# Kernel optimization log

Measured on AMD Instinct MI355X. Metric: run time of the kernel, lower is better.

## Reference

```python
import jax, jax.numpy as jnp
import numpy as np

B, N, WIDTH, HEADS = 4, 2048, 1024, 16
HEAD_DIM = WIDTH // HEADS  # 64


def setup_inputs() -> dict:
    key = jax.random.key(0)
    k1, k2, k3 = jax.random.split(key, 3)
    x = jax.random.normal(k1, (B, N, WIDTH), dtype=jnp.float32)
    # Linear weights stored as [in, out] (torch stores [out, in]; math y = x @ W_in_out + b)
    w_qkv = jax.random.normal(k2, (WIDTH, 3 * WIDTH), dtype=jnp.float32) * (1.0 / np.sqrt(WIDTH))
    b_qkv = jnp.zeros((3 * WIDTH,), dtype=jnp.float32)
    w_proj = jax.random.normal(k3, (WIDTH, WIDTH), dtype=jnp.float32) * (1.0 / np.sqrt(WIDTH))
    b_proj = jnp.zeros((WIDTH,), dtype=jnp.float32)
    return {"x": x, "w_qkv": w_qkv, "b_qkv": b_qkv, "w_proj": w_proj, "b_proj": b_proj}


def reference(x, w_qkv, b_qkv, w_proj, b_proj):
    bs, n_ctx, width = x.shape
    qkv = x @ w_qkv + b_qkv                      # [b, n, 3*width]
    attn_ch = HEAD_DIM                            # width // heads
    scale = 1.0 / np.sqrt(np.sqrt(attn_ch))       # 1/sqrt(sqrt(d)) applied to q and k
    qkv = qkv.reshape(bs, n_ctx, HEADS, 3 * attn_ch)
    q, k, v = jnp.split(qkv, 3, axis=-1)          # each [b, n, h, d]
    weight = jnp.einsum('bthc,bshc->bhts', q * scale, k * scale)
    weight = jax.nn.softmax(weight, axis=-1)
    out = jnp.einsum('bhts,bshc->bthc', weight, v).reshape(bs, n_ctx, -1)
    return out @ w_proj + b_proj
```

## Files before the change

kernel.cpp:

```cpp
#include <hip/hip_runtime.h>

typedef __attribute__((ext_vector_type(8))) short bf16x8;
typedef __attribute__((ext_vector_type(4))) float f32x4;
typedef __attribute__((ext_vector_type(8))) unsigned short u16x8;
typedef __attribute__((ext_vector_type(4))) unsigned short u16x4;
typedef __attribute__((ext_vector_type(2))) unsigned u32x2;

__device__ __forceinline__ unsigned short f2bf(float f) {
  unsigned u = __builtin_bit_cast(unsigned, f);
  return (unsigned short)((u + 0x7fffu + ((u >> 16) & 1u)) >> 16);
}

__device__ __forceinline__ unsigned cvt_pk_bf16(float lo, float hi) {
  unsigned r;
  asm("v_cvt_pk_bf16_f32 %0, %1, %2" : "=v"(r) : "v"(lo), "v"(hi));
  return r;
}

__device__ __forceinline__ void gl_lds16(const void* g, void* l) {
  __builtin_amdgcn_global_load_lds((const __attribute__((address_space(1))) unsigned*)g,
                                   (__attribute__((address_space(3))) unsigned*)l, 16, 0, 0);
}

__global__ __launch_bounds__(256) void k_cvt(const float* __restrict__ x,
                                             unsigned short* __restrict__ xb) {
  int i = blockIdx.x * 256 + threadIdx.x;
  const float4* s = (const float4*)x;
  float4 a = s[2 * i], b = s[2 * i + 1];
  u16x8 o;
  o[0] = f2bf(a.x); o[1] = f2bf(a.y); o[2] = f2bf(a.z); o[3] = f2bf(a.w);
  o[4] = f2bf(b.x); o[5] = f2bf(b.y); o[6] = f2bf(b.z); o[7] = f2bf(b.w);
  *(u16x8*)(xb + 8 * (size_t)i) = o;
}

__global__ __launch_bounds__(256) void k_wT(const float* __restrict__ w,
                                            unsigned short* __restrict__ wT,
                                            int Nn, int Kk) {
  __shared__ float tile[32][33];
  const int k0 = blockIdx.x * 32, n0 = blockIdx.y * 32;
  const int t = threadIdx.x;
  const int i = t >> 3, j = (t & 7) * 4;
  float4 v = *(const float4*)(w + (size_t)(k0 + i) * Nn + n0 + j);
  tile[i][j] = v.x; tile[i][j + 1] = v.y; tile[i][j + 2] = v.z; tile[i][j + 3] = v.w;
  __syncthreads();
  const int n = i, k4 = j;
  u16x4 o;
  o[0] = f2bf(tile[k4 + 0][n]); o[1] = f2bf(tile[k4 + 1][n]);
  o[2] = f2bf(tile[k4 + 2][n]); o[3] = f2bf(tile[k4 + 3][n]);
  *(u16x4*)(wT + (size_t)(n0 + n) * Kk + k0 + k4) = o;
}

template <int EPI>
__global__ __launch_bounds__(256) void k_gemm(const unsigned short* __restrict__ A,
                                              const unsigned short* __restrict__ Bt,
                                              const float* __restrict__ bias, int Nx,
                                              int MT,
                                              float* __restrict__ outF,
                                              unsigned short* __restrict__ Qb,
                                              unsigned short* __restrict__ Kb,
                                              unsigned short* __restrict__ Vb) {
  __shared__ unsigned short As[128 * 32];
  __shared__ unsigned short Bs[128 * 32];
  const int t = threadIdx.x;
  const int nwg = gridDim.x;
  const int wg = (blockIdx.x & 7) * (nwg >> 3) + (blockIdx.x >> 3);
  const int brow = (wg % MT) * 128, bcol = (wg / MT) * 128;
  const int lane = t & 63, wid = t >> 6;
  const int wr = (wid >> 1) * 64, wc = (wid & 1) * 64;
  const int g = lane >> 4, qr = lane & 15;
  const f32x4 fzero = {0.f, 0.f, 0.f, 0.f};
  f32x4 acc[4][4];
#pragma unroll
  for (int i = 0; i < 4; ++i)
#pragma unroll
    for (int n = 0; n < 4; ++n) acc[i][n] = fzero;
  const unsigned short* Ag = A + (size_t)(brow + (t >> 2)) * 1024 + (t & 3) * 8;
  const unsigned short* Bg = Bt + (size_t)(bcol + (t >> 2)) * 1024 + (t & 3) * 8;
  unsigned short* Asl = As + t * 8;
  unsigned short* Bsl = Bs + t * 8;
  for (int kt = 0; kt < 32; ++kt) {
    const int k0 = kt * 32;
    gl_lds16(Ag + k0, Asl);
    gl_lds16(Ag + 64 * 1024 + k0, Asl + 2048);
    gl_lds16(Bg + k0, Bsl);
    gl_lds16(Bg + 64 * 1024 + k0, Bsl + 2048);
    __syncthreads();
    bf16x8 a[4], b[4];
#pragma unroll
    for (int i = 0; i < 4; ++i) a[i] = *(const bf16x8*)&As[(wr + i * 16 + qr) * 32 + g * 8];
#pragma unroll
    for (int n = 0; n < 4; ++n) b[n] = *(const bf16x8*)&Bs[(wc + n * 16 + qr) * 32 + g * 8];
#pragma unroll
    for (int i = 0; i < 4; ++i)
#pragma unroll
      for (int n = 0; n < 4; ++n)
        acc[i][n] = __builtin_amdgcn_mfma_f32_16x16x32_bf16(a[i], b[n], acc[i][n], 0, 0, 0);
    __syncthreads();
  }
#pragma unroll
  for (int i = 0; i < 4; ++i) {
#pragma unroll
    for (int n = 0; n < 4; ++n) {
      const int col = bcol + wc + n * 16 + qr;
      const float bv = bias[col];
      float v4[4];
#pragma unroll
      for (int r = 0; r < 4; ++r) v4[r] = acc[i][n][r] + bv;
      const int row0 = brow + wr + i * 16 + g * 4;
      if constexpr (EPI == 0) {
#pragma unroll
        for (int r = 0; r < 4; ++r) outF[(size_t)(row0 + r) * Nx + col] = v4[r];
      } else {
        const int bb = row0 >> 11, tkn0 = row0 & 2047;
        const unsigned c = (unsigned)col;
        const unsigned h = c / 192u;
        const unsigned rem = c - h * 192u;
        const unsigned which = rem >> 6, d = rem & 63u;
        if (which == 2u) {
          u16x4 pk;
#pragma unroll
          for (int r = 0; r < 4; ++r) pk[r] = f2bf(v4[r]);
          *(u16x4*)&Vb[(size_t)(((unsigned)bb * 16u + h) * 64u + d) * 2048u + (unsigned)tkn0] = pk;
        } else {
          const float sc = (which == 0u) ? (0.35355339059327373f * 1.4426950408889634f)
                                         : 0.35355339059327373f;
          unsigned short* dst = (which == 0u) ? Qb : Kb;
#pragma unroll
          for (int r = 0; r < 4; ++r)
            dst[(size_t)(((unsigned)bb * 16u + h) * 2048u + (unsigned)(tkn0 + r)) * 64u + d] =
                f2bf(v4[r] * sc);
        }
      }
    }
  }
}

__global__ __launch_bounds__(512, 4) void k_attn(const unsigned short* __restrict__ Qb,
                                                 const unsigned short* __restrict__ Kb,
                                                 const unsigned short* __restrict__ Vt,
                                                 unsigned short* __restrict__ Ao) {
  __shared__ unsigned short Kl[2][64][64];
  __shared__ unsigned short Vl[2][64][64];
  __shared__ unsigned short Pl[8][2][16][72];
  const int bid = blockIdx.x;
  const int bh = (bid & 7) * 8 + ((bid >> 3) & 7);
  const int qt = bid >> 6;
  const int t = threadIdx.x, lane = t & 63, w = t >> 6;
  const int g = lane >> 4, q = lane & 15;
  const int q0 = qt * 256 + w * 32;
  const unsigned short* Qbase = Qb + ((size_t)bh * 2048 + q0) * 64;
  const char* Kg = (const char*)(Kb + (size_t)bh * 2048 * 64);
  const char* Vg = (const char*)(Vt + (size_t)bh * 64 * 2048);
  const int lr = lane >> 3, lc = lane & 7;
  const int swz = (lc ^ lr) << 4;
  const char* Ksrc = Kg + (size_t)(8 * w + lr) * 128 + swz;
  const char* Vsrc = Vg + (size_t)(8 * w + lr) * 4096 + swz;
  unsigned short* Kd[2], *Vd[2];
  Kd[0] = &Kl[0][8 * w][0] + lane * 8;
  Kd[1] = &Kl[1][8 * w][0] + lane * 8;
  Vd[0] = &Vl[0][8 * w][0] + lane * 8;
  Vd[1] = &Vl[1][8 * w][0] + lane * 8;

#define STAGE(buf, it_)                              \
  do {                                               \
    gl_lds16(Ksrc + (size_t)(it_) * 8192, Kd[buf]);  \
    gl_lds16(Vsrc + (size_t)(it_) * 128, Vd[buf]);   \
  } while (0)

  bf16x8 qf[2][2];
#pragma unroll
  for (int G = 0; G < 2; ++G)
#pragma unroll
    for (int h = 0; h < 2; ++h)
      qf[G][h] = *(const bf16x8*)(Qbase + (size_t)(G * 16 + q) * 64 + h * 32 + g * 8);
  const f32x4 fzero = {0.f, 0.f, 0.f, 0.f};
  f32x4 o0[4], o1[4];
#pragma unroll
  for (int i = 0; i < 4; ++i) { o0[i] = fzero; o1[i] = fzero; }
  float l0 = 0.f, l1 = 0.f;

  STAGE(0, 0);
  __syncthreads();

  for (int it = 0; it < 32; ++it) {
    const int cur = it & 1;
    if (it < 31) STAGE(cur ^ 1, it + 1);
    f32x4 s0[4], s1[4];
    __builtin_amdgcn_s_setprio(1);
#pragma unroll
    for (int kf = 0; kf < 4; ++kf) {
      const int row = kf * 16 + q;
      const char* kp = (const char*)&Kl[cur][row][0];
      const int sw = (row & 7) << 4;
      bf16x8 kaL = *(const bf16x8*)(kp + ((g * 16) ^ sw));
      bf16x8 kaH = *(const bf16x8*)(kp + ((64 + g * 16) ^ sw));
      s0[kf] = __builtin_amdgcn_mfma_f32_16x16x32_bf16(kaL, qf[0][0], fzero, 0, 0, 0);
      s0[kf] = __builtin_amdgcn_mfma_f32_16x16x32_bf16(kaH, qf[0][1], s0[kf], 0, 0, 0);
      s1[kf] = __builtin_amdgcn_mfma_f32_16x16x32_bf16(kaL, qf[1][0], fzero, 0, 0, 0);
      s1[kf] = __builtin_amdgcn_mfma_f32_16x16x32_bf16(kaH, qf[1][1], s1[kf], 0, 0, 0);
    }
    __builtin_amdgcn_s_setprio(0);
    {
      unsigned short* Pw = &Pl[w][0][q][0];
#pragma unroll
      for (int kf = 0; kf < 4; ++kf) {
        const float e0 = __builtin_amdgcn_exp2f(s0[kf][0]);
        const float e1 = __builtin_amdgcn_exp2f(s0[kf][1]);
        const float e2 = __builtin_amdgcn_exp2f(s0[kf][2]);
        const float e3 = __builtin_amdgcn_exp2f(s0[kf][3]);
        l0 += (e0 + e1) + (e2 + e3);
        u32x2 pk;
        pk[0] = cvt_pk_bf16(e0, e1);
        pk[1] = cvt_pk_bf16(e2, e3);
        *(u32x2*)(Pw + (8 * kf + 2 * g) * 2) = pk;
      }
    }
    {
      unsigned short* Pw = &Pl[w][1][q][0];
#pragma unroll
      for (int kf = 0; kf < 4; ++kf) {
        const float e0 = __builtin_amdgcn_exp2f(s1[kf][0]);
        const float e1 = __builtin_amdgcn_exp2f(s1[kf][1]);
        const float e2 = __builtin_amdgcn_exp2f(s1[kf][2]);
        const float e3 = __builtin_amdgcn_exp2f(s1[kf][3]);
        l1 += (e0 + e1) + (e2 + e3);
        u32x2 pk;
        pk[0] = cvt_pk_bf16(e0, e1);
        pk[1] = cvt_pk_bf16(e2, e3);
        *(u32x2*)(Pw + (8 * kf + 2 * g) * 2) = pk;
      }
    }
    asm volatile("" ::: "memory");
    const bf16x8 pa00 = *(const bf16x8*)&Pl[w][0][q][g * 8];
    const bf16x8 pa01 = *(const bf16x8*)&Pl[w][0][q][32 + g * 8];
    const bf16x8 pa10 = *(const bf16x8*)&Pl[w][1][q][g * 8];
    const bf16x8 pa11 = *(const bf16x8*)&Pl[w][1][q][32 + g * 8];
    __builtin_amdgcn_s_setprio(1);
#pragma unroll
    for (int dblk = 0; dblk < 4; ++dblk) {
      const int row = dblk * 16 + q;
      const char* vp = (const char*)&Vl[cur][row][0];
      const int sw = (row & 7) << 4;
      bf16x8 vL = *(const bf16x8*)(vp + ((g * 16) ^ sw));
      bf16x8 vH = *(const bf16x8*)(vp + ((64 + g * 16) ^ sw));
      o0[dblk] = __builtin_amdgcn_mfma_f32_16x16x32_bf16(vL, pa00, o0[dblk], 0, 0, 0);
      o0[dblk] = __builtin_amdgcn_mfma_f32_16x16x32_bf16(vH, pa01, o0[dblk], 0, 0, 0);
      o1[dblk] = __builtin_amdgcn_mfma_f32_16x16x32_bf16(vL, pa10, o1[dblk], 0, 0, 0);
      o1[dblk] = __builtin_amdgcn_mfma_f32_16x16x32_bf16(vH, pa11, o1[dblk], 0, 0, 0);
    }
    __builtin_amdgcn_s_setprio(0);
    __syncthreads();
  }
#undef STAGE
  l0 += __shfl_xor(l0, 16); l0 += __shfl_xor(l0, 32);
  l1 += __shfl_xor(l1, 16); l1 += __shfl_xor(l1, 32);
  const float li0 = 1.0f / l0, li1 = 1.0f / l1;
  const int bb = bh >> 4, hh = bh & 15;
  {
    unsigned short* ob = Ao + ((size_t)bb * 2048 + q0 + q) * 1024 + hh * 64 + 4 * g;
#pragma unroll
    for (int dblk = 0; dblk < 4; ++dblk) {
      u16x4 pk;
#pragma unroll
      for (int r = 0; r < 4; ++r) pk[r] = f2bf(o0[dblk][r] * li0);
      *(u16x4*)(ob + dblk * 16) = pk;
    }
  }
  {
    unsigned short* ob = Ao + ((size_t)bb * 2048 + q0 + 16 + q) * 1024 + hh * 64 + 4 * g;
#pragma unroll
    for (int dblk = 0; dblk < 4; ++dblk) {
      u16x4 pk;
#pragma unroll
      for (int r = 0; r < 4; ++r) pk[r] = f2bf(o1[dblk][r] * li1);
      *(u16x4*)(ob + dblk * 16) = pk;
    }
  }
}

extern "C" void kernel_launch(void* const* d_in, const int* in_sizes, int n_in,
                              void* d_out, int out_size, void* d_ws, size_t ws_size,
                              hipStream_t stream) {
  const float* x = (const float*)d_in[0];
  const float* w_qkv = (const float*)d_in[1];
  const float* b_qkv = (const float*)d_in[2];
  const float* w_proj = (const float*)d_in[3];
  const float* b_proj = (const float*)d_in[4];
  float* out = (float*)d_out;
  char* ws = (char*)d_ws;
  unsigned short* xb = (unsigned short*)(ws);
  unsigned short* wqkvT = (unsigned short*)(ws + 16777216);
  unsigned short* wprojT = (unsigned short*)(ws + 23068672);
  unsigned short* Qb = (unsigned short*)(ws + 25165824);
  unsigned short* Kb = (unsigned short*)(ws + 41943040);
  unsigned short* Vt = (unsigned short*)(ws + 58720256);
  unsigned short* Ao = xb;

  hipLaunchKernelGGL(k_cvt, dim3(4096), dim3(256), 0, stream, x, xb);
  hipLaunchKernelGGL(k_wT, dim3(32, 96), dim3(256), 0, stream, w_qkv, wqkvT, 3072, 1024);
  hipLaunchKernelGGL(k_wT, dim3(32, 32), dim3(256), 0, stream, w_proj, wprojT, 1024, 1024);
  hipLaunchKernelGGL((k_gemm<1>), dim3(1536), dim3(256), 0, stream,
                     xb, wqkvT, b_qkv, 3072, 64, (float*)nullptr, Qb, Kb, Vt);
  hipLaunchKernelGGL(k_attn, dim3(512), dim3(512), 0, stream, Qb, Kb, Vt, Ao);
  hipLaunchKernelGGL((k_gemm<0>), dim3(512), dim3(256), 0, stream,
                     Ao, wprojT, b_proj, 1024, 64, out,
                     (unsigned short*)nullptr, (unsigned short*)nullptr, (unsigned short*)nullptr);
}
```

Measured before the change: 193.0 us.

## Feed softmax probabilities to PV MFMA from registers via 16x16x16 instructions

Removes the per-wave LDS round trip for the probability matrix P. The QK^T accumulator layout is reused directly as the B operand of 16x16x16 bf16 MFMAs, and V is read as 4-element slices matching that layout. This saves LDS writes and reads plus the LDS footprint for P, but doubles the number of PV MFMA issues, which use the older half-K instruction, and drops the priority hints around them.

```diff
diff --git a/kernel.cpp b/kernel.cpp
--- a/kernel.cpp
+++ b/kernel.cpp
@@ -1,6 +1,7 @@
 #include <hip/hip_runtime.h>
 
 typedef __attribute__((ext_vector_type(8))) short bf16x8;
+typedef __attribute__((ext_vector_type(4))) short bf16x4;
 typedef __attribute__((ext_vector_type(4))) float f32x4;
 typedef __attribute__((ext_vector_type(8))) unsigned short u16x8;
 typedef __attribute__((ext_vector_type(4))) unsigned short u16x4;
@@ -15,6 +16,18 @@
   unsigned r;
   asm("v_cvt_pk_bf16_f32 %0, %1, %2" : "=v"(r) : "v"(lo), "v"(hi));
   return r;
+}
+
+__device__ __forceinline__ f32x4 mfma16(bf16x4 a, bf16x4 b, f32x4 c) {
+#if __has_builtin(__builtin_amdgcn_mfma_f32_16x16x16bf16_1k)
+  return __builtin_amdgcn_mfma_f32_16x16x16bf16_1k(a, b, c, 0, 0, 0);
+#elif __has_builtin(__builtin_amdgcn_mfma_f32_16x16x16_bf16)
+  return __builtin_amdgcn_mfma_f32_16x16x16_bf16(a, b, c, 0, 0, 0);
+#else
+  f32x4 d;
+  asm("v_mfma_f32_16x16x16_bf16 %0, %1, %2, %3" : "=v"(d) : "v"(a), "v"(b), "v"(c));
+  return d;
+#endif
 }
 
 __device__ __forceinline__ void gl_lds16(const void* g, void* l) {
@@ -141,7 +154,6 @@
                                                  unsigned short* __restrict__ Ao) {
   __shared__ unsigned short Kl[2][64][64];
   __shared__ unsigned short Vl[2][64][64];
-  __shared__ unsigned short Pl[8][2][16][72];
   const int bid = blockIdx.x;
   const int bh = (bid & 7) * 8 + ((bid >> 3) & 7);
   const int qt = bid >> 6;
@@ -200,55 +212,37 @@
       s1[kf] = __builtin_amdgcn_mfma_f32_16x16x32_bf16(kaH, qf[1][1], s1[kf], 0, 0, 0);
     }
     __builtin_amdgcn_s_setprio(0);
-    {
-      unsigned short* Pw = &Pl[w][0][q][0];
-#pragma unroll
-      for (int kf = 0; kf < 4; ++kf) {
-        const float e0 = __builtin_amdgcn_exp2f(s0[kf][0]);
-        const float e1 = __builtin_amdgcn_exp2f(s0[kf][1]);
-        const float e2 = __builtin_amdgcn_exp2f(s0[kf][2]);
-        const float e3 = __builtin_amdgcn_exp2f(s0[kf][3]);
-        l0 += (e0 + e1) + (e2 + e3);
-        u32x2 pk;
-        pk[0] = cvt_pk_bf16(e0, e1);
-        pk[1] = cvt_pk_bf16(e2, e3);
-        *(u32x2*)(Pw + (8 * kf + 2 * g) * 2) = pk;
+#pragma unroll
+    for (int kf = 0; kf < 4; ++kf) {
+      const float e00 = __builtin_amdgcn_exp2f(s0[kf][0]);
+      const float e01 = __builtin_amdgcn_exp2f(s0[kf][1]);
+      const float e02 = __builtin_amdgcn_exp2f(s0[kf][2]);
+      const float e03 = __builtin_amdgcn_exp2f(s0[kf][3]);
+      l0 += (e00 + e01) + (e02 + e03);
+      u32x2 pk0;
+      pk0[0] = cvt_pk_bf16(e00, e01);
+      pk0[1] = cvt_pk_bf16(e02, e03);
+      const bf16x4 pf0 = __builtin_bit_cast(bf16x4, pk0);
+      const float e10 = __builtin_amdgcn_exp2f(s1[kf][0]);
+      const float e11 = __builtin_amdgcn_exp2f(s1[kf][1]);
+      const float e12 = __builtin_amdgcn_exp2f(s1[kf][2]);
+      const float e13 = __builtin_amdgcn_exp2f(s1[kf][3]);
+      l1 += (e10 + e11) + (e12 + e13);
+      u32x2 pk1;
+      pk1[0] = cvt_pk_bf16(e10, e11);
+      pk1[1] = cvt_pk_bf16(e12, e13);
+      const bf16x4 pf1 = __builtin_bit_cast(bf16x4, pk1);
+      const int off = 32 * kf + 8 * g;
+#pragma unroll
+      for (int dblk = 0; dblk < 4; ++dblk) {
+        const int row = dblk * 16 + q;
+        const char* vp = (const char*)&Vl[cur][row][0];
+        const int sw = (row & 7) << 4;
+        const bf16x4 vf = *(const bf16x4*)(vp + (off ^ sw));
+        o0[dblk] = mfma16(vf, pf0, o0[dblk]);
+        o1[dblk] = mfma16(vf, pf1, o1[dblk]);
       }
     }
-    {
-      unsigned short* Pw = &Pl[w][1][q][0];
-#pragma unroll
-      for (int kf = 0; kf < 4; ++kf) {
-        const float e0 = __builtin_amdgcn_exp2f(s1[kf][0]);
-        const float e1 = __builtin_amdgcn_exp2f(s1[kf][1]);
-        const float e2 = __builtin_amdgcn_exp2f(s1[kf][2]);
-        const float e3 = __builtin_amdgcn_exp2f(s1[kf][3]);
-        l1 += (e0 + e1) + (e2 + e3);
-        u32x2 pk;
-        pk[0] = cvt_pk_bf16(e0, e1);
-        pk[1] = cvt_pk_bf16(e2, e3);
-        *(u32x2*)(Pw + (8 * kf + 2 * g) * 2) = pk;
-      }
-    }
-    asm volatile("" ::: "memory");
-    const bf16x8 pa00 = *(const bf16x8*)&Pl[w][0][q][g * 8];
-    const bf16x8 pa01 = *(const bf16x8*)&Pl[w][0][q][32 + g * 8];
-    const bf16x8 pa10 = *(const bf16x8*)&Pl[w][1][q][g * 8];
-    const bf16x8 pa11 = *(const bf16x8*)&Pl[w][1][q][32 + g * 8];
-    __builtin_amdgcn_s_setprio(1);
-#pragma unroll
-    for (int dblk = 0; dblk < 4; ++dblk) {
-      const int row = dblk * 16 + q;
-      const char* vp = (const char*)&Vl[cur][row][0];
-      const int sw = (row & 7) << 4;
-      bf16x8 vL = *(const bf16x8*)(vp + ((g * 16) ^ sw));
-      bf16x8 vH = *(const bf16x8*)(vp + ((64 + g * 16) ^ sw));
-      o0[dblk] = __builtin_amdgcn_mfma_f32_16x16x32_bf16(vL, pa00, o0[dblk], 0, 0, 0);
-      o0[dblk] = __builtin_amdgcn_mfma_f32_16x16x32_bf16(vH, pa01, o0[dblk], 0, 0, 0);
-      o1[dblk] = __builtin_amdgcn_mfma_f32_16x16x32_bf16(vL, pa10, o1[dblk], 0, 0, 0);
-      o1[dblk] = __builtin_amdgcn_mfma_f32_16x16x32_bf16(vH, pa11, o1[dblk], 0, 0, 0);
-    }
-    __builtin_amdgcn_s_setprio(0);
     __syncthreads();
   }
 #undef STAGE
```

Measured after the change: 195.4 us. No clear change (+1.2%).

## Double GEMM K-tile to 64 with XOR-swizzled LDS layout

Applied to the files above, without the earlier changes.

The GEMM main loop now stages a 64-wide K slice per iteration instead of 32, halving the number of barrier pairs and loop iterations. The LDS tile uses an XOR swizzle on 16-byte chunks, applied to the global source address, to avoid bank conflicts on the wider row stride. This doubles LDS use per block and adds some index arithmetic. The attention kernel only gains alignment attributes.

```diff
diff --git a/kernel.cpp b/kernel.cpp
--- a/kernel.cpp
+++ b/kernel.cpp
@@ -59,8 +59,8 @@
                                               unsigned short* __restrict__ Qb,
                                               unsigned short* __restrict__ Kb,
                                               unsigned short* __restrict__ Vb) {
-  __shared__ unsigned short As[128 * 32];
-  __shared__ unsigned short Bs[128 * 32];
+  __shared__ __attribute__((aligned(16))) unsigned short As[128 * 64];
+  __shared__ __attribute__((aligned(16))) unsigned short Bs[128 * 64];
   const int t = threadIdx.x;
   const int nwg = gridDim.x;
   const int wg = (blockIdx.x & 7) * (nwg >> 3) + (blockIdx.x >> 3);
@@ -74,27 +74,59 @@
   for (int i = 0; i < 4; ++i)
 #pragma unroll
     for (int n = 0; n < 4; ++n) acc[i][n] = fzero;
-  const unsigned short* Ag = A + (size_t)(brow + (t >> 2)) * 1024 + (t & 3) * 8;
-  const unsigned short* Bg = Bt + (size_t)(bcol + (t >> 2)) * 1024 + (t & 3) * 8;
+  const int strow = t >> 3;
+  const int swz8 = ((t & 7) ^ (strow & 7)) << 3;
+  const unsigned short* Ag = A + (size_t)(brow + strow) * 1024 + swz8;
+  const unsigned short* Bg = Bt + (size_t)(bcol + strow) * 1024 + swz8;
   unsigned short* Asl = As + t * 8;
   unsigned short* Bsl = Bs + t * 8;
-  for (int kt = 0; kt < 32; ++kt) {
-    const int k0 = kt * 32;
+  for (int kt = 0; kt < 16; ++kt) {
+    const int k0 = kt * 64;
     gl_lds16(Ag + k0, Asl);
-    gl_lds16(Ag + 64 * 1024 + k0, Asl + 2048);
+    gl_lds16(Ag + 32 * 1024 + k0, Asl + 2048);
+    gl_lds16(Ag + 64 * 1024 + k0, Asl + 4096);
+    gl_lds16(Ag + 96 * 1024 + k0, Asl + 6144);
     gl_lds16(Bg + k0, Bsl);
-    gl_lds16(Bg + 64 * 1024 + k0, Bsl + 2048);
+    gl_lds16(Bg + 32 * 1024 + k0, Bsl + 2048);
+    gl_lds16(Bg + 64 * 1024 + k0, Bsl + 4096);
+    gl_lds16(Bg + 96 * 1024 + k0, Bsl + 6144);
     __syncthreads();
-    bf16x8 a[4], b[4];
-#pragma unroll
-    for (int i = 0; i < 4; ++i) a[i] = *(const bf16x8*)&As[(wr + i * 16 + qr) * 32 + g * 8];
-#pragma unroll
-    for (int n = 0; n < 4; ++n) b[n] = *(const bf16x8*)&Bs[(wc + n * 16 + qr) * 32 + g * 8];
-#pragma unroll
-    for (int i = 0; i < 4; ++i)
-#pragma unroll
-      for (int n = 0; n < 4; ++n)
-        acc[i][n] = __builtin_amdgcn_mfma_f32_16x16x32_bf16(a[i], b[n], acc[i][n], 0, 0, 0);
+    {
+      bf16x8 a[4], b[4];
+#pragma unroll
+      for (int i = 0; i < 4; ++i) {
+        const int r = wr + i * 16 + qr;
+        a[i] = *(const bf16x8*)&As[r * 64 + ((g ^ (r & 7)) << 3)];
+      }
+#pragma unroll
+      for (int n = 0; n < 4; ++n) {
+        const int r = wc + n * 16 + qr;
+        b[n] = *(const bf16x8*)&Bs[r * 64 + ((g ^ (r & 7)) << 3)];
+      }
+#pragma unroll
+      for (int i = 0; i < 4; ++i)
+#pragma unroll
+        for (int n = 0; n < 4; ++n)
+          acc[i][n] = __builtin_amdgcn_mfma_f32_16x16x32_bf16(a[i], b[n], acc[i][n], 0, 0, 0);
+    }
+    {
+      bf16x8 a[4], b[4];
+#pragma unroll
+      for (int i = 0; i < 4; ++i) {
+        const int r = wr + i * 16 + qr;
+        a[i] = *(const bf16x8*)&As[r * 64 + (((4 + g) ^ (r & 7)) << 3)];
+      }
+#pragma unroll
+      for (int n = 0; n < 4; ++n) {
+        const int r = wc + n * 16 + qr;
+        b[n] = *(const bf16x8*)&Bs[r * 64 + (((4 + g) ^ (r & 7)) << 3)];
+      }
+#pragma unroll
+      for (int i = 0; i < 4; ++i)
+#pragma unroll
+        for (int n = 0; n < 4; ++n)
+          acc[i][n] = __builtin_amdgcn_mfma_f32_16x16x32_bf16(a[i], b[n], acc[i][n], 0, 0, 0);
+    }
     __syncthreads();
   }
 #pragma unroll
@@ -139,9 +171,9 @@
                                                  const unsigned short* __restrict__ Kb,
                                                  const unsigned short* __restrict__ Vt,
                                                  unsigned short* __restrict__ Ao) {
-  __shared__ unsigned short Kl[2][64][64];
-  __shared__ unsigned short Vl[2][64][64];
-  __shared__ unsigned short Pl[8][2][16][72];
+  __shared__ __attribute__((aligned(16))) unsigned short Kl[2][64][64];
+  __shared__ __attribute__((aligned(16))) unsigned short Vl[2][64][64];
+  __shared__ __attribute__((aligned(16))) unsigned short Pl[8][2][16][72];
   const int bid = blockIdx.x;
   const int bh = (bid & 7) * 8 + ((bid >> 3) & 7);
   const int qt = bid >> 6;
```

New measurement: 189.8 us. Within noise of the previous version (-1.6%).

## Triple-buffer GEMM LDS loads with swizzle and fuse prep kernels

Applied to the files above, without the earlier changes.

The GEMM kernel now uses a 3-stage LDS ring fed by async global_load_lds. It waits on vmcnt instead of taking two __syncthreads per k-step, and raises wave priority around the MFMA block. The LDS layout is XOR-swizzled to cut bank conflicts, and the tile-to-workgroup mapping is changed for L2 locality. The three conversion and transpose kernels are merged into one launch to remove launch overhead. The trade-off is more LDS per block, and the single barrier per stage relies on the prefetch distance leaving enough slack to avoid overwriting a buffer still being read.

```diff
diff --git a/kernel.cpp b/kernel.cpp
--- a/kernel.cpp
+++ b/kernel.cpp
@@ -22,23 +22,32 @@
                                    (__attribute__((address_space(3))) unsigned*)l, 16, 0, 0);
 }
 
-__global__ __launch_bounds__(256) void k_cvt(const float* __restrict__ x,
-                                             unsigned short* __restrict__ xb) {
-  int i = blockIdx.x * 256 + threadIdx.x;
-  const float4* s = (const float4*)x;
-  float4 a = s[2 * i], b = s[2 * i + 1];
-  u16x8 o;
-  o[0] = f2bf(a.x); o[1] = f2bf(a.y); o[2] = f2bf(a.z); o[3] = f2bf(a.w);
-  o[4] = f2bf(b.x); o[5] = f2bf(b.y); o[6] = f2bf(b.z); o[7] = f2bf(b.w);
-  *(u16x8*)(xb + 8 * (size_t)i) = o;
-}
-
-__global__ __launch_bounds__(256) void k_wT(const float* __restrict__ w,
-                                            unsigned short* __restrict__ wT,
-                                            int Nn, int Kk) {
+__global__ __launch_bounds__(256) void k_prep(const float* __restrict__ x,
+                                              unsigned short* __restrict__ xb,
+                                              const float* __restrict__ wq,
+                                              unsigned short* __restrict__ wqT,
+                                              const float* __restrict__ wp,
+                                              unsigned short* __restrict__ wpT) {
   __shared__ float tile[32][33];
-  const int k0 = blockIdx.x * 32, n0 = blockIdx.y * 32;
+  const int bx = blockIdx.x;
   const int t = threadIdx.x;
+  if (bx < 4096) {
+    const int i = bx * 256 + t;
+    const float4* s = (const float4*)x;
+    float4 a = s[2 * i], b = s[2 * i + 1];
+    u16x8 o;
+    o[0] = f2bf(a.x); o[1] = f2bf(a.y); o[2] = f2bf(a.z); o[3] = f2bf(a.w);
+    o[4] = f2bf(b.x); o[5] = f2bf(b.y); o[6] = f2bf(b.z); o[7] = f2bf(b.w);
+    *(u16x8*)(xb + 8 * (size_t)i) = o;
+    return;
+  }
+  const int b = bx - 4096;
+  const float* w;
+  unsigned short* wT;
+  int Nn, bb;
+  if (b < 3072) { w = wq; wT = wqT; Nn = 3072; bb = b; }
+  else          { w = wp; wT = wpT; Nn = 1024; bb = b - 3072; }
+  const int k0 = (bb & 31) * 32, n0 = (bb >> 5) * 32;
   const int i = t >> 3, j = (t & 7) * 4;
   float4 v = *(const float4*)(w + (size_t)(k0 + i) * Nn + n0 + j);
   tile[i][j] = v.x; tile[i][j + 1] = v.y; tile[i][j + 2] = v.z; tile[i][j + 3] = v.w;
@@ -47,24 +56,23 @@
   u16x4 o;
   o[0] = f2bf(tile[k4 + 0][n]); o[1] = f2bf(tile[k4 + 1][n]);
   o[2] = f2bf(tile[k4 + 2][n]); o[3] = f2bf(tile[k4 + 3][n]);
-  *(u16x4*)(wT + (size_t)(n0 + n) * Kk + k0 + k4) = o;
+  *(u16x4*)(wT + (size_t)(n0 + n) * 1024 + k0 + k4) = o;
 }
 
 template <int EPI>
 __global__ __launch_bounds__(256) void k_gemm(const unsigned short* __restrict__ A,
                                               const unsigned short* __restrict__ Bt,
                                               const float* __restrict__ bias, int Nx,
-                                              int MT,
                                               float* __restrict__ outF,
                                               unsigned short* __restrict__ Qb,
                                               unsigned short* __restrict__ Kb,
                                               unsigned short* __restrict__ Vb) {
-  __shared__ unsigned short As[128 * 32];
-  __shared__ unsigned short Bs[128 * 32];
+  __shared__ __attribute__((aligned(16))) unsigned short As[3][128 * 32];
+  __shared__ __attribute__((aligned(16))) unsigned short Bs[3][128 * 32];
   const int t = threadIdx.x;
-  const int nwg = gridDim.x;
-  const int wg = (blockIdx.x & 7) * (nwg >> 3) + (blockIdx.x >> 3);
-  const int brow = (wg % MT) * 128, bcol = (wg / MT) * 128;
+  const int jj = blockIdx.x >> 3;
+  const int brow = ((blockIdx.x & 7) * 8 + (jj & 7)) * 128;
+  const int bcol = (jj >> 3) * 128;
   const int lane = t & 63, wid = t >> 6;
   const int wr = (wid >> 1) * 64, wc = (wid & 1) * 64;
   const int g = lane >> 4, qr = lane & 15;
@@ -74,29 +82,52 @@
   for (int i = 0; i < 4; ++i)
 #pragma unroll
     for (int n = 0; n < 4; ++n) acc[i][n] = fzero;
-  const unsigned short* Ag = A + (size_t)(brow + (t >> 2)) * 1024 + (t & 3) * 8;
-  const unsigned short* Bg = Bt + (size_t)(bcol + (t >> 2)) * 1024 + (t & 3) * 8;
-  unsigned short* Asl = As + t * 8;
-  unsigned short* Bsl = Bs + t * 8;
+  const int srow = t >> 2;
+  const int sg = (t & 3) ^ (srow & 3);
+  const unsigned short* Ag0 = A + (size_t)(brow + srow) * 1024 + sg * 8;
+  const unsigned short* Bg0 = Bt + (size_t)(bcol + srow) * 1024 + sg * 8;
+
+#define STAGE(s_, kt_)                                        \
+  do {                                                        \
+    const int koff = (kt_) * 32;                              \
+    gl_lds16(Ag0 + koff, &As[s_][t * 8]);                     \
+    gl_lds16(Ag0 + 64 * 1024 + koff, &As[s_][2048 + t * 8]);  \
+    gl_lds16(Bg0 + koff, &Bs[s_][t * 8]);                     \
+    gl_lds16(Bg0 + 64 * 1024 + koff, &Bs[s_][2048 + t * 8]);  \
+  } while (0)
+
+  STAGE(0, 0);
+  STAGE(1, 1);
   for (int kt = 0; kt < 32; ++kt) {
-    const int k0 = kt * 32;
-    gl_lds16(Ag + k0, Asl);
-    gl_lds16(Ag + 64 * 1024 + k0, Asl + 2048);
-    gl_lds16(Bg + k0, Bsl);
-    gl_lds16(Bg + 64 * 1024 + k0, Bsl + 2048);
-    __syncthreads();
+    const int s = kt % 3;
+    if (kt < 31) {
+      asm volatile("s_waitcnt vmcnt(4)" ::: "memory");
+    } else {
+      asm volatile("s_waitcnt vmcnt(0)" ::: "memory");
+    }
+    __builtin_amdgcn_s_barrier();
+    __builtin_amdgcn_sched_barrier(0);
     bf16x8 a[4], b[4];
 #pragma unroll
-    for (int i = 0; i < 4; ++i) a[i] = *(const bf16x8*)&As[(wr + i * 16 + qr) * 32 + g * 8];
-#pragma unroll
-    for (int n = 0; n < 4; ++n) b[n] = *(const bf16x8*)&Bs[(wc + n * 16 + qr) * 32 + g * 8];
+    for (int i = 0; i < 4; ++i) {
+      const int r = wr + i * 16 + qr;
+      a[i] = *(const bf16x8*)&As[s][r * 32 + ((g ^ (r & 3)) << 3)];
+    }
+#pragma unroll
+    for (int n = 0; n < 4; ++n) {
+      const int r = wc + n * 16 + qr;
+      b[n] = *(const bf16x8*)&Bs[s][r * 32 + ((g ^ (r & 3)) << 3)];
+    }
+    __builtin_amdgcn_s_setprio(1);
 #pragma unroll
     for (int i = 0; i < 4; ++i)
 #pragma unroll
       for (int n = 0; n < 4; ++n)
         acc[i][n] = __builtin_amdgcn_mfma_f32_16x16x32_bf16(a[i], b[n], acc[i][n], 0, 0, 0);
-    __syncthreads();
-  }
+    __builtin_amdgcn_s_setprio(0);
+    if (kt < 30) STAGE((kt + 2) % 3, kt + 2);
+  }
+#undef STAGE
 #pragma unroll
   for (int i = 0; i < 4; ++i) {
 #pragma unroll
@@ -139,9 +170,9 @@
                                                  const unsigned short* __restrict__ Kb,
                                                  const unsigned short* __restrict__ Vt,
                                                  unsigned short* __restrict__ Ao) {
-  __shared__ unsigned short Kl[2][64][64];
-  __shared__ unsigned short Vl[2][64][64];
-  __shared__ unsigned short Pl[8][2][16][72];
+  __shared__ __attribute__((aligned(16))) unsigned short Kl[2][64][64];
+  __shared__ __attribute__((aligned(16))) unsigned short Vl[2][64][64];
+  __shared__ __attribute__((aligned(16))) unsigned short Pl[8][2][16][72];
   const int bid = blockIdx.x;
   const int bh = (bid & 7) * 8 + ((bid >> 3) & 7);
   const int qt = bid >> 6;
@@ -296,13 +327,12 @@
   unsigned short* Vt = (unsigned short*)(ws + 58720256);
   unsigned short* Ao = xb;
 
-  hipLaunchKernelGGL(k_cvt, dim3(4096), dim3(256), 0, stream, x, xb);
-  hipLaunchKernelGGL(k_wT, dim3(32, 96), dim3(256), 0, stream, w_qkv, wqkvT, 3072, 1024);
-  hipLaunchKernelGGL(k_wT, dim3(32, 32), dim3(256), 0, stream, w_proj, wprojT, 1024, 1024);
+  hipLaunchKernelGGL(k_prep, dim3(8192), dim3(256), 0, stream,
+                     x, xb, w_qkv, wqkvT, w_proj, wprojT);
   hipLaunchKernelGGL((k_gemm<1>), dim3(1536), dim3(256), 0, stream,
-                     xb, wqkvT, b_qkv, 3072, 64, (float*)nullptr, Qb, Kb, Vt);
+                     xb, wqkvT, b_qkv, 3072, (float*)nullptr, Qb, Kb, Vt);
   hipLaunchKernelGGL(k_attn, dim3(512), dim3(512), 0, stream, Qb, Kb, Vt, Ao);
   hipLaunchKernelGGL((k_gemm<0>), dim3(512), dim3(256), 0, stream,
-                     Ao, wprojT, b_proj, 1024, 64, out,
+                     Ao, wprojT, b_proj, 1024, out,
                      (unsigned short*)nullptr, (unsigned short*)nullptr, (unsigned short*)nullptr);
 }
```

After: 178.5 us. -7.5%, faster.
